# Kernel tuning notes

Measured on AMD Instinct MI355X. Metric: run time of the kernel, lower is better.

The kernel has to match this reference:

```python
import jax, jax.numpy as jnp
import numpy as np
from jax import lax

N = 5000            # number of detections
FEAT = 1024         # last-layer feature dim; 1024 + 9 engineered feats = indim 1033
DIMS = [FEAT + 9, 1000, 600, 300, 150, 1]
IOU_THRESH = 0.5
EPS = 2.220446049250313e-16  # sys.float_info.epsilon


def setup_inputs() -> dict:
    key = jax.random.key(0)
    ks = jax.random.split(key, 8 + 3 * len(DIMS))
    H, W = 800.0, 1333.0
    cx = jax.random.uniform(ks[0], (N,), minval=0.0, maxval=W)
    cy = jax.random.uniform(ks[1], (N,), minval=0.0, maxval=H)
    bw = jax.random.uniform(ks[2], (N,), minval=20.0, maxval=250.0)
    bh = jax.random.uniform(ks[3], (N,), minval=20.0, maxval=250.0)
    x1 = jnp.clip(cx - bw / 2, 0.0, W - 2)
    y1 = jnp.clip(cy - bh / 2, 0.0, H - 2)
    x2 = jnp.clip(cx + bw / 2, x1 + 1, W)
    y2 = jnp.clip(cy + bh / 2, y1 + 1, H)
    inp = {
        'multi_bboxes': jnp.stack([x1, y1, x2, y2], axis=1),
        'cls_score': jax.random.uniform(ks[4], (N, 2)),
        'last_layer_feats': jax.random.normal(ks[5], (N, FEAT)),
        'img_shape': jnp.array([H, W], jnp.float32),
    }
    # PermEqui2_mean params: Gamma (weight+bias) and Lambda (weight only)
    ki = 6
    for i, (din, dout) in enumerate(zip(DIMS[:-1], DIMS[1:])):
        s = 1.0 / np.sqrt(din)
        inp[f'Wg{i+1}'] = jax.random.uniform(ks[ki], (dout, din), minval=-s, maxval=s); ki += 1
        inp[f'bg{i+1}'] = jax.random.uniform(ks[ki], (dout,), minval=-s, maxval=s); ki += 1
        inp[f'Wl{i+1}'] = jax.random.uniform(ks[ki], (dout, din), minval=-s, maxval=s); ki += 1
    return inp


def _greedy_cluster(ious, thresh):
    # Sequential greedy IoU clustering (NMS-like). assign[i] = index of cluster seed.
    n = ious.shape[0]

    def step(carry, inp):
        is_c, assign = carry
        j, row = inp
        seed = is_c[j]
        hit = row > thresh
        member = seed & hit & is_c
        assign = jnp.where(member, j, assign)
        is_c = is_c & ~(seed & hit)
        return (is_c, assign), None

    init = (jnp.ones(n, bool), jnp.zeros(n, jnp.int32))
    (_, assign), _ = lax.scan(step, init, (jnp.arange(n, dtype=jnp.int32), ious))
    return assign


def _forward(multi_bboxes, cls_score, last_layer_feats, img_shape, params):
    n = multi_bboxes.shape[0]
    scores = cls_score[:, 1]
    order = jnp.argsort(-scores)
    scores = scores[order]
    bboxes = multi_bboxes[order]
    feats = last_layer_feats[order]

    x1, y1, x2, y2 = bboxes[:, 0], bboxes[:, 1], bboxes[:, 2], bboxes[:, 3]
    # pairwise IoU with the +1 pixel convention from bbox_overlaps
    iw = jnp.clip(jnp.minimum(x2[:, None], x2[None, :]) - jnp.maximum(x1[:, None], x1[None, :]) + 1, 0)
    ih = jnp.clip(jnp.minimum(y2[:, None], y2[None, :]) - jnp.maximum(y1[:, None], y1[None, :]) + 1, 0)
    area = (x2 - x1 + 1) * (y2 - y1 + 1)
    overlap = iw * ih
    ious = overlap / (area[:, None] + area[None, :] - overlap)

    assign = _greedy_cluster(lax.stop_gradient(ious), IOU_THRESH)
    counts = jax.ops.segment_sum(jnp.ones(n, jnp.float32), assign, num_segments=n)
    cden = jnp.maximum(counts, 1.0)

    Himg, Wimg = img_shape[0], img_shape[1]
    # source double-normalizes: width = (x2/W - x1/W)/W, height = (y2/H - y1/H)/H
    width = (x2 / Wimg - x1 / Wimg) / Wimg
    height = (y2 / Himg - y1 / Himg) / Himg
    areaf = width * height
    ar = width / (height + EPS)
    x = jnp.concatenate([
        bboxes, feats,
        width[:, None], height[:, None], ar[:, None], areaf[:, None], scores[:, None],
    ], axis=1)  # [n, 1033]

    def perm_equi(x, Wg, bg, Wl):
        # xm = per-set mean; x*Gamma^T + b - (xm*Lambda^T), gathered back per box
        xm = jax.ops.segment_sum(x, assign, num_segments=n) / cden[:, None]
        return x @ Wg.T + bg - (xm @ Wl.T)[assign]

    for i in range(5):
        x = jax.nn.elu(perm_equi(x, params[f'Wg{i+1}'], params[f'bg{i+1}'], params[f'Wl{i+1}']))

    # source skips singleton sets (nonzero().squeeze() -> 0-dim): mask them out
    valid = counts[assign] >= 2.0
    return jnp.where(valid[:, None], x, 0.0)  # [n, 1] per-box set logits


def reference(multi_bboxes, cls_score, last_layer_feats, img_shape,
              Wg1, bg1, Wl1, Wg2, bg2, Wl2, Wg3, bg3, Wl3,
              Wg4, bg4, Wl4, Wg5, bg5, Wl5):
    params = {'Wg1': Wg1, 'bg1': bg1, 'Wl1': Wl1, 'Wg2': Wg2, 'bg2': bg2, 'Wl2': Wl2,
              'Wg3': Wg3, 'bg3': bg3, 'Wl3': Wl3, 'Wg4': Wg4, 'bg4': bg4, 'Wl4': Wl4,
              'Wg5': Wg5, 'bg5': bg5, 'Wl5': Wl5}
    return _forward(multi_bboxes, cls_score, last_layer_feats, img_shape, params)
```

## Files before the change

### kernel.cpp

```cpp
#include <hip/hip_runtime.h>
#include <cstdint>
#include <cstddef>

#define N_BOX 5000
#define NW    80
#define LDX   1040
#define LDZ   2048
#define LDYM  1000
#define LDW   1040
#define LDAB  2080
#define NCHUNK ((N_BOX + 63) / 64)
#define RT    ((N_BOX + 255) / 256)

typedef short bf16x8 __attribute__((ext_vector_type(8)));
typedef float f32x4v __attribute__((ext_vector_type(4)));
typedef unsigned short u16x8 __attribute__((ext_vector_type(8)));

__device__ __forceinline__ float fence_f(float x) { asm volatile("" : "+v"(x)); return x; }

__device__ __forceinline__ unsigned short f2bf(float x) {
    unsigned u = __builtin_bit_cast(unsigned, x);
    unsigned r = (u + 0x7FFFu + ((u >> 16) & 1u)) >> 16;
    return (unsigned short)r;
}
__device__ __forceinline__ float bf2f(unsigned short h) {
    unsigned u = ((unsigned)h) << 16;
    return __builtin_bit_cast(float, u);
}

__global__ void rank_partial_kernel(const float* __restrict__ cls, int* __restrict__ rank) {
    __shared__ float sj[256];
    int t = threadIdx.x;
    int jbase = blockIdx.y * 256;
    int jg = jbase + t;
    sj[t] = (jg < N_BOX) ? cls[2 * jg + 1] : 0.0f;
    __syncthreads();
    int i = blockIdx.x * 256 + t;
    if (i >= N_BOX) return;
    float si = cls[2 * i + 1];
    int jmax = (N_BOX - jbase < 256) ? (N_BOX - jbase) : 256;
    int r = 0;
    for (int k = 0; k < jmax; ++k) {
        float sjv = sj[k];
        int j = jbase + k;
        r += (sjv > si) || (sjv == si && j < i);
    }
    atomicAdd(&rank[i], r);
}

__global__ void rank_scatter_kernel(const int* __restrict__ rank, int* __restrict__ ord) {
    int i = blockIdx.x * blockDim.x + threadIdx.x;
    if (i < N_BOX) ord[rank[i]] = i;
}

__global__ void gather_kernel(const float* __restrict__ bb, const float* __restrict__ cls,
                              const float* __restrict__ feats, const float* __restrict__ img,
                              const int* __restrict__ ord,
                              float* __restrict__ X0, float* __restrict__ sb) {
    int r = blockIdx.x;
    int i = ord[r];
    float x1 = bb[4 * i + 0], y1 = bb[4 * i + 1], x2 = bb[4 * i + 2], y2 = bb[4 * i + 3];
    float H = img[0], W = img[1];
    float sc = cls[2 * i + 1];
    if (threadIdx.x == 0) {
        sb[0 * N_BOX + r] = x1;
        sb[1 * N_BOX + r] = y1;
        sb[2 * N_BOX + r] = x2;
        sb[3 * N_BOX + r] = y2;
        sb[4 * N_BOX + r] = (x2 - x1 + 1.0f) * (y2 - y1 + 1.0f);
        sb[5 * N_BOX + r] = sc;
    }
    float width  = (x2 / W - x1 / W) / W;
    float height = (y2 / H - y1 / H) / H;
    float ar     = width / (height + 2.220446049250313e-16f);
    float areaf  = width * height;
    float* row = X0 + (size_t)r * LDX;
    for (int o = threadIdx.x; o < LDX; o += blockDim.x) {
        float v;
        if (o < 4)          v = (o == 0) ? x1 : (o == 1) ? y1 : (o == 2) ? x2 : y2;
        else if (o < 1028)  v = feats[(size_t)i * 1024 + (o - 4)];
        else if (o == 1028) v = width;
        else if (o == 1029) v = height;
        else if (o == 1030) v = ar;
        else if (o == 1031) v = areaf;
        else if (o == 1032) v = sc;
        else                v = 0.0f;
        row[o] = v;
    }
}

__global__ void mask_kernel(const float* __restrict__ sb, unsigned long long* __restrict__ mask,
                            unsigned long long* __restrict__ diag, int* __restrict__ counts) {
    int j = blockIdx.x;
    if (threadIdx.x == 0) counts[j] = 0;
    const float* X1 = sb;
    const float* Y1 = sb + N_BOX;
    const float* X2 = sb + 2 * N_BOX;
    const float* Y2 = sb + 3 * N_BOX;
    const float* AR = sb + 4 * N_BOX;
    float xj1 = X1[j], yj1 = Y1[j], xj2 = X2[j], yj2 = Y2[j], aj = AR[j];
    int lane = threadIdx.x & 63;
    int wave = threadIdx.x >> 6;
    int nwav = blockDim.x >> 6;
    int dw = j >> 6;
    for (int w = wave; w < NW; w += nwav) {
        int i = w * 64 + lane;
        bool pred = false;
        if (i < N_BOX) {
            float iw = fmaxf(fminf(xj2, X2[i]) - fmaxf(xj1, X1[i]) + 1.0f, 0.0f);
            float ih = fmaxf(fminf(yj2, Y2[i]) - fmaxf(yj1, Y1[i]) + 1.0f, 0.0f);
            float ov = fence_f(iw * ih);
            float denom = fence_f((aj + AR[i]) - ov);
            pred = (ov / denom) > 0.5f;
        }
        unsigned long long b = __ballot(pred);
        if (lane == 0) {
            mask[(size_t)j * NW + w] = b;
            if (w == dw) diag[j] = b;
        }
    }
}

__device__ __forceinline__ void nms_body(const unsigned long long* __restrict__ mask,
                                         const unsigned long long* __restrict__ diag,
                                         unsigned long long* __restrict__ keep,
                                         unsigned long long* supp,
                                         unsigned long long* keep_sh,
                                         unsigned long long* rem_sh,
                                         unsigned long long* kb_sh) {
    int tid = threadIdx.x;
    int l = tid & 63;
    int w = tid >> 6;
    if (tid < 80) supp[tid] = 0ULL;
    unsigned long long dg = 0ULL, dg_next = 0ULL;
    if (w == 0) dg = diag[l];
    __syncthreads();
    for (int c = 0; c < NCHUNK; ++c) {
        if (w == 0) {
            unsigned long long curv = supp[c];
            unsigned clo = __builtin_amdgcn_readfirstlane((unsigned)curv);
            unsigned chi = __builtin_amdgcn_readfirstlane((unsigned)(curv >> 32));
            unsigned long long cur = ((unsigned long long)chi << 32) | clo;
            int jmax = (N_BOX - c * 64 < 64) ? (N_BOX - c * 64) : 64;
            unsigned long long valid = (jmax >= 64) ? ~0ULL : ((1ULL << jmax) - 1ULL);
            unsigned long long rem = ~cur & valid;
            if (l == 0) *rem_sh = rem;
        }
        __syncthreads();
        unsigned long long rem0 = *rem_sh;
        unsigned long long a0 = 0, a1 = 0, a2 = 0, a3 = 0, a4 = 0;
        unsigned long long b0 = 0, b1 = 0, b2 = 0, b3 = 0, b4 = 0;
        unsigned mym = 0;
        int base = (w - 1) * 5;
        if (w > 0) {
            mym = (base < 64) ? (unsigned)((rem0 >> base) & 31ULL) : 0u;
            const unsigned long long* rowp = mask + (size_t)(c * 64 + base) * NW;
            if (mym & 1u)  { a0 = rowp[0 * NW + l]; b0 = (l < 16) ? rowp[0 * NW + 64 + l] : 0ULL; }
            if (mym & 2u)  { a1 = rowp[1 * NW + l]; b1 = (l < 16) ? rowp[1 * NW + 64 + l] : 0ULL; }
            if (mym & 4u)  { a2 = rowp[2 * NW + l]; b2 = (l < 16) ? rowp[2 * NW + 64 + l] : 0ULL; }
            if (mym & 8u)  { a3 = rowp[3 * NW + l]; b3 = (l < 16) ? rowp[3 * NW + 64 + l] : 0ULL; }
            if (mym & 16u) { a4 = rowp[4 * NW + l]; b4 = (l < 16) ? rowp[4 * NW + 64 + l] : 0ULL; }
        } else {
            if (c + 1 < NCHUNK) dg_next = diag[(size_t)(c + 1) * 64 + l];
            unsigned rlo = __builtin_amdgcn_readfirstlane((unsigned)rem0);
            unsigned rhi = __builtin_amdgcn_readfirstlane((unsigned)(rem0 >> 32));
            unsigned long long remS = ((unsigned long long)rhi << 32) | rlo;
            unsigned long long kb = 0ULL;
            while (remS) {
                int jj = __builtin_ctzll(remS);
                kb |= 1ULL << jj;
                unsigned dlo = __builtin_amdgcn_readlane((unsigned)dg, jj);
                unsigned dhi = __builtin_amdgcn_readlane((unsigned)(dg >> 32), jj);
                unsigned long long dj = ((unsigned long long)dhi << 32) | dlo;
                remS &= ~dj;
                remS &= ~(1ULL << jj);
            }
            if (l == 0) { *kb_sh = kb; keep_sh[c] = kb; }
        }
        __syncthreads();
        if (w > 0 && mym) {
            unsigned long long kb = *kb_sh;
            unsigned kw = ((unsigned)((kb >> base) & 31ULL)) & mym;
            if (kw & 1u)  { atomicOr(&supp[l], a0); if (l < 16) atomicOr(&supp[64 + l], b0); }
            if (kw & 2u)  { atomicOr(&supp[l], a1); if (l < 16) atomicOr(&supp[64 + l], b1); }
            if (kw & 4u)  { atomicOr(&supp[l], a2); if (l < 16) atomicOr(&supp[64 + l], b2); }
            if (kw & 8u)  { atomicOr(&supp[l], a3); if (l < 16) atomicOr(&supp[64 + l], b3); }
            if (kw & 16u) { atomicOr(&supp[l], a4); if (l < 16) atomicOr(&supp[64 + l], b4); }
        }
        if (w == 0) dg = dg_next;
        __syncthreads();
    }
    if (tid < NCHUNK) keep[tid] = keep_sh[tid];
}

__global__ __launch_bounds__(1024) void nms_scan_kernel(const unsigned long long* __restrict__ mask,
                                                        const unsigned long long* __restrict__ diag,
                                                        unsigned long long* __restrict__ keep) {
    __shared__ unsigned long long supp[80];
    __shared__ unsigned long long keep_sh[NCHUNK];
    __shared__ unsigned long long rem_sh;
    __shared__ unsigned long long kb_sh;
    nms_body(mask, diag, keep, supp, keep_sh, &rem_sh, &kb_sh);
}

__device__ __forceinline__ void wconv_row(const float* __restrict__ Wg, const float* __restrict__ Wl,
                                          unsigned short* __restrict__ B2, int n, int tid2,
                                          int dout, int din, int K16) {
    unsigned short* dst = B2 + (size_t)n * LDAB;
    int K2 = 2 * K16;
    if (n >= 2 * dout) {
        for (int k = tid2; k < K2; k += 256) dst[k] = 0;
        return;
    }
    const float* src = (n < dout) ? (Wg + (size_t)n * din) : (Wl + (size_t)(n - dout) * din);
    for (int k = tid2; k < K2; k += 256) {
        int ks = (k >= K16) ? (k - K16) : k;
        float x = (ks < din) ? src[ks] : 0.0f;
        dst[k] = f2bf(x);
    }
}

__global__ __launch_bounds__(1024) void nms_gemm_fused(const unsigned long long* __restrict__ mask,
                                                       const unsigned long long* __restrict__ diag,
                                                       unsigned long long* __restrict__ keep,
                                                       const unsigned short* __restrict__ A2,
                                                       const unsigned short* __restrict__ B2,
                                                       float* __restrict__ C, int KT, int Nn,
                                                       int MTiles,
                                                       const float* __restrict__ X0,
                                                       float* __restrict__ E9, float* __restrict__ W9,
                                                       const float* __restrict__ Wg1, const float* __restrict__ Wl1,
                                                       const float* __restrict__ Wg0full, const float* __restrict__ Wl0full,
                                                       unsigned short* __restrict__ B2_1,
                                                       const float* __restrict__ Wg2, const float* __restrict__ Wl2,
                                                       unsigned short* __restrict__ B2_2,
                                                       const float* __restrict__ Wg3, const float* __restrict__ Wl3,
                                                       unsigned short* __restrict__ B2_3) {
    __shared__ __align__(16) unsigned short AsBuf[2 * 8192];
    __shared__ __align__(16) unsigned short BsBuf[2 * 8192];
    int tid = threadIdx.x;
    int b = blockIdx.x;
    if (b == 0) {
        unsigned long long* supp    = (unsigned long long*)AsBuf;
        unsigned long long* keep_sh = supp + 80;
        unsigned long long* rem_sh  = keep_sh + NCHUNK;
        unsigned long long* kb_sh   = rem_sh + 1;
        nms_body(mask, diag, keep, supp, keep_sh, rem_sh, kb_sh);
        return;
    }
    int NG = MTiles * 8;
    if (b <= NG) {
        int t = b - 1;
        size_t bm = (size_t)(t % MTiles) * 256;
        size_t bn = (size_t)(t / MTiles) * 256;
        int lane = tid & 63;
        int wavef = tid >> 6;
        int wr = wavef >> 2, wc = wavef & 3;

        f32x4v acc[4][4];
#pragma unroll
        for (int i = 0; i < 4; ++i)
#pragma unroll
            for (int j = 0; j < 4; ++j) acc[i][j] = (f32x4v){0.f, 0.f, 0.f, 0.f};

        const unsigned short* gA = A2 + (bm + wavef * 16 + (lane & 15)) * (size_t)LDAB + (lane >> 4) * 8;
        const unsigned short* gB = B2 + (bn + wavef * 16 + (lane & 15)) * (size_t)LDAB + (lane >> 4) * 8;
        unsigned ldsoff = (unsigned)((wavef * 64 + lane) * 16);

#define FSTAGE(T, BUF)                                                                             \
        {                                                                                          \
            size_t ko = (size_t)(T) * 32;                                                          \
            __builtin_amdgcn_global_load_lds(                                                      \
                (const __attribute__((address_space(1))) void*)(gA + ko),                          \
                (__attribute__((address_space(3))) void*)((char*)AsBuf + (BUF) * 16384 + ldsoff),  \
                16, 0, 0);                                                                         \
            __builtin_amdgcn_global_load_lds(                                                      \
                (const __attribute__((address_space(1))) void*)(gB + ko),                          \
                (__attribute__((address_space(3))) void*)((char*)BsBuf + (BUF) * 16384 + ldsoff),  \
                16, 0, 0);                                                                         \
        }

        FSTAGE(0, 0);
        for (int kt = 0; kt < KT; ++kt) {
            int cur = kt & 1;
            if (kt + 1 < KT) {
                FSTAGE(kt + 1, cur ^ 1);
                asm volatile("s_waitcnt vmcnt(2)" ::: "memory");
            } else {
                asm volatile("s_waitcnt vmcnt(0)" ::: "memory");
            }
            asm volatile("s_barrier" ::: "memory");
            bf16x8 af[4], bf[4];
#pragma unroll
            for (int f4 = 0; f4 < 4; ++f4) {
                af[f4] = *(const bf16x8*)((const char*)AsBuf + cur * 16384 + ((wr * 4 + f4) * 64 + lane) * 16);
                bf[f4] = *(const bf16x8*)((const char*)BsBuf + cur * 16384 + ((wc * 4 + f4) * 64 + lane) * 16);
            }
#pragma unroll
            for (int i = 0; i < 4; ++i)
#pragma unroll
                for (int j = 0; j < 4; ++j)
                    acc[i][j] = __builtin_amdgcn_mfma_f32_16x16x32_bf16(af[i], bf[j], acc[i][j], 0, 0, 0);
            asm volatile("s_barrier" ::: "memory");
        }
#undef FSTAGE

#pragma unroll
        for (int i = 0; i < 4; ++i) {
            int r0 = (int)bm + wr * 64 + i * 16 + (lane >> 4) * 4;
#pragma unroll
            for (int j = 0; j < 4; ++j) {
                int col = (int)bn + wc * 64 + j * 16 + (lane & 15);
                if (col < Nn) {
#pragma unroll
                    for (int e = 0; e < 4; ++e) {
                        int r = r0 + e;
                        if (r < N_BOX) C[(size_t)r * LDZ + col] = acc[i][j][e];
                    }
                }
            }
        }
        return;
    }
    int rb = b - 1 - NG;
    const int cq[9] = {0, 1, 2, 3, 1028, 1029, 1030, 1031, 1032};
    if (rb < 5) {
        int r = rb * 1024 + tid;
        if (r < 5120) {
            float* dst = E9 + (size_t)r * 12;
#pragma unroll
            for (int q = 0; q < 9; ++q) dst[q] = (r < N_BOX) ? X0[(size_t)r * LDX + cq[q]] : 0.0f;
            dst[9] = dst[10] = dst[11] = 0.0f;
        }
        return;
    }
    rb -= 5;
    if (rb < 2) {
        int n = rb * 1024 + tid;
        if (n < 2048) {
            float* dst = W9 + (size_t)n * 12;
            const float* src = (n < 1000) ? (Wg0full + (size_t)n * 1033)
                             : (n < 2000) ? (Wl0full + (size_t)(n - 1000) * 1033) : nullptr;
#pragma unroll
            for (int q = 0; q < 9; ++q) dst[q] = src ? src[cq[q]] : 0.0f;
            dst[9] = dst[10] = dst[11] = 0.0f;
        }
        return;
    }
    rb -= 2;
    int rowl = tid >> 8;
    int tid2 = tid & 255;
    if (rb < 320) {
        int n = rb * 4 + rowl;
        if (n < 1280) wconv_row(Wg1, Wl1, B2_1, n, tid2, 600, 1000, 1008);
        return;
    }
    rb -= 320;
    if (rb < 160) {
        int n = rb * 4 + rowl;
        if (n < 640) wconv_row(Wg2, Wl2, B2_2, n, tid2, 300, 600, 608);
        return;
    }
    rb -= 160;
    {
        int n = rb * 4 + rowl;
        if (n < 384) wconv_row(Wg3, Wl3, B2_3, n, tid2, 150, 300, 304);
        return;
    }
}

__global__ void z9_assign_kernel(float* __restrict__ Z, const float* __restrict__ E9,
                                 const float* __restrict__ W9, int Nn,
                                 const unsigned long long* __restrict__ mask,
                                 const unsigned long long* __restrict__ keep,
                                 int* __restrict__ assign, int* __restrict__ counts) {
    int b = blockIdx.x;
    if (b < N_BOX) {
        int r = b;
        float e[9];
#pragma unroll
        for (int q = 0; q < 9; ++q) e[q] = E9[(size_t)r * 12 + q];
        for (int o = threadIdx.x; o < Nn; o += blockDim.x) {
            const float* w = W9 + (size_t)o * 12;
            float s = 0.0f;
#pragma unroll
            for (int q = 0; q < 9; ++q) s += e[q] * w[q];
            Z[(size_t)r * LDZ + o] += s;
        }
        return;
    }
    int i = (b - N_BOX) * 256 + threadIdx.x;
    if (i >= N_BOX) return;
    for (int w = 0; w < NCHUNK; ++w) {
        unsigned long long m = mask[(size_t)i * NW + w] & keep[w];
        if (m) {
            int j = w * 64 + __builtin_ctzll(m);
            assign[i] = j;
            atomicAdd(&counts[j], 1);
            return;
        }
    }
}

__global__ void assign_kernel(const unsigned long long* __restrict__ mask,
                              const unsigned long long* __restrict__ keep,
                              int* __restrict__ assign, int* __restrict__ counts) {
    int i = blockIdx.x * blockDim.x + threadIdx.x;
    if (i >= N_BOX) return;
    for (int w = 0; w < NCHUNK; ++w) {
        unsigned long long m = mask[(size_t)i * NW + w] & keep[w];
        if (m) {
            int j = w * 64 + __builtin_ctzll(m);
            assign[i] = j;
            atomicAdd(&counts[j], 1);
            return;
        }
    }
}

__global__ __launch_bounds__(1024) void scan_kernel(const int* __restrict__ counts, int* __restrict__ offs) {
    __shared__ int part[1024];
    int t = threadIdx.x;
    int base = t * 5;
    int c[5];
    int s = 0;
#pragma unroll
    for (int k = 0; k < 5; ++k) {
        int idx = base + k;
        c[k] = (idx < N_BOX) ? counts[idx] : 0;
        s += c[k];
    }
    part[t] = s;
    __syncthreads();
    for (int d = 1; d < 1024; d <<= 1) {
        int v = part[t];
        int u = (t >= d) ? part[t - d] : 0;
        __syncthreads();
        part[t] = v + u;
        __syncthreads();
    }
    int run = (t > 0) ? part[t - 1] : 0;
#pragma unroll
    for (int k = 0; k < 5; ++k) {
        int idx = base + k;
        if (idx < N_BOX) offs[idx] = run;
        run += c[k];
    }
}

__global__ void rankscatter_kernel(const int* __restrict__ assign, const int* __restrict__ offs,
                                   int* __restrict__ members) {
    __shared__ int a[N_BOX];
    int tid = threadIdx.x;
    for (int t = tid; t < N_BOX; t += blockDim.x) a[t] = assign[t];
    __syncthreads();
    int i = blockIdx.x * blockDim.x + tid;
    if (i >= N_BOX) return;
    int ai = a[i];
    int r = 0;
    for (int k = 0; k < i; ++k) r += (a[k] == ai);
    members[offs[ai] + r] = i;
}

__global__ void xconv_kernel(const float* __restrict__ X, unsigned short* __restrict__ A2,
                             int K16eff, int colOff) {
    int r = blockIdx.x;
    unsigned short* dst = A2 + (size_t)r * LDAB;
    int K2 = 2 * K16eff;
    int nk8 = K2 >> 3;
    if (r >= N_BOX) {
        for (int k8 = threadIdx.x; k8 < nk8; k8 += blockDim.x) {
            u16x8 z;
#pragma unroll
            for (int j = 0; j < 8; ++j) z[j] = 0;
            *(u16x8*)(dst + (k8 << 3)) = z;
        }
        return;
    }
    const float* src = X + (size_t)r * LDX + colOff;
    for (int k8 = threadIdx.x; k8 < nk8; k8 += blockDim.x) {
        int kb = k8 << 3;
        bool lo = (kb >= K16eff);
        int ks = lo ? (kb - K16eff) : kb;
        u16x8 out;
#pragma unroll
        for (int j = 0; j < 8; ++j) {
            float x = src[ks + j];
            unsigned short ah = f2bf(x);
            out[j] = lo ? f2bf(x - bf2f(ah)) : ah;
        }
        *(u16x8*)(dst + kb) = out;
    }
}

__global__ void wconv_kernel(const float* __restrict__ Wg, const float* __restrict__ Wl,
                             unsigned short* __restrict__ B2, int dout, int din_src,
                             int din_eff, int colOff, int K16eff) {
    int n = blockIdx.x;
    unsigned short* dst = B2 + (size_t)n * LDAB;
    int K2 = 2 * K16eff;
    if (n >= 2 * dout) {
        for (int k = threadIdx.x; k < K2; k += blockDim.x) dst[k] = 0;
        return;
    }
    const float* src = (n < dout) ? (Wg + (size_t)n * din_src) : (Wl + (size_t)(n - dout) * din_src);
    for (int k = threadIdx.x; k < K2; k += blockDim.x) {
        int ks = (k >= K16eff) ? (k - K16eff) : k;
        float x = (ks < din_eff) ? src[colOff + ks] : 0.0f;
        dst[k] = f2bf(x);
    }
}

__global__ __launch_bounds__(256, 4) void gemm_mfma(const unsigned short* __restrict__ A2,
                                                    const unsigned short* __restrict__ B2,
                                                    float* __restrict__ C, int KT, int Nn) {
    __shared__ unsigned short AsBuf[2 * 4096];
    __shared__ unsigned short BsBuf[2 * 4096];
    int tid = threadIdx.x;
    int lane = tid & 63;
    int wave = tid >> 6;
    int wr = wave >> 1, wc = wave & 1;
    size_t bm = (size_t)blockIdx.x * 128;
    size_t bn = (size_t)blockIdx.y * 128;

    f32x4v acc[4][4];
#pragma unroll
    for (int i = 0; i < 4; ++i)
#pragma unroll
        for (int j = 0; j < 4; ++j) acc[i][j] = (f32x4v){0.f, 0.f, 0.f, 0.f};

    const unsigned short* gA[2];
    const unsigned short* gB[2];
    unsigned ldsoff[2];
#pragma unroll
    for (int q = 0; q < 2; ++q) {
        int f = q * 4 + wave;
        int grow = f * 16 + (lane & 15);
        int gcol = (lane >> 4) * 8;
        gA[q] = A2 + (bm + grow) * (size_t)LDAB + gcol;
        gB[q] = B2 + (bn + grow) * (size_t)LDAB + gcol;
        ldsoff[q] = (unsigned)((f * 64 + lane) * 16);
    }

#define STAGE(T, BUF)                                                                              \
    {                                                                                              \
        size_t ko = (size_t)(T) * 32;                                                              \
        _Pragma("unroll") for (int q = 0; q < 2; ++q) {                                            \
            __builtin_amdgcn_global_load_lds(                                                      \
                (const __attribute__((address_space(1))) void*)(gA[q] + ko),                       \
                (__attribute__((address_space(3))) void*)((char*)AsBuf + (BUF) * 8192 + ldsoff[q]),\
                16, 0, 0);                                                                         \
            __builtin_amdgcn_global_load_lds(                                                      \
                (const __attribute__((address_space(1))) void*)(gB[q] + ko),                       \
                (__attribute__((address_space(3))) void*)((char*)BsBuf + (BUF) * 8192 + ldsoff[q]),\
                16, 0, 0);                                                                         \
        }                                                                                          \
    }

    STAGE(0, 0);
    for (int kt = 0; kt < KT; ++kt) {
        int cur = kt & 1;
        if (kt + 1 < KT) {
            STAGE(kt + 1, cur ^ 1);
            asm volatile("s_waitcnt vmcnt(4)" ::: "memory");
        } else {
            asm volatile("s_waitcnt vmcnt(0)" ::: "memory");
        }
        asm volatile("s_barrier" ::: "memory");
        bf16x8 af[4], bf[4];
#pragma unroll
        for (int f4 = 0; f4 < 4; ++f4) {
            af[f4] = *(const bf16x8*)((const char*)AsBuf + cur * 8192 + ((wr * 4 + f4) * 64 + lane) * 16);
            bf[f4] = *(const bf16x8*)((const char*)BsBuf + cur * 8192 + ((wc * 4 + f4) * 64 + lane) * 16);
        }
#pragma unroll
        for (int i = 0; i < 4; ++i)
#pragma unroll
            for (int j = 0; j < 4; ++j)
                acc[i][j] = __builtin_amdgcn_mfma_f32_16x16x32_bf16(af[i], bf[j], acc[i][j], 0, 0, 0);
        asm volatile("s_barrier" ::: "memory");
    }
#undef STAGE

#pragma unroll
    for (int i = 0; i < 4; ++i) {
        int r0 = (int)bm + wr * 64 + i * 16 + (lane >> 4) * 4;
#pragma unroll
        for (int j = 0; j < 4; ++j) {
            int col = (int)bn + wc * 64 + j * 16 + (lane & 15);
            if (col < Nn) {
#pragma unroll
                for (int e = 0; e < 4; ++e) {
                    int r = r0 + e;
                    if (r < N_BOX) C[(size_t)r * LDZ + col] = acc[i][j][e];
                }
            }
        }
    }
}

__global__ void wcat_kernel(const float* __restrict__ Wg, const float* __restrict__ Wl,
                            float* __restrict__ Wc, int dout, int din, int K16) {
    int row = blockIdx.x;
    const float* src = (row < dout) ? (Wg + (size_t)row * din) : (Wl + (size_t)(row - dout) * din);
    float* dst = Wc + (size_t)row * LDW;
    for (int k = threadIdx.x; k < K16; k += blockDim.x)
        dst[k] = (k < din) ? src[k] : 0.0f;
}

__global__ __launch_bounds__(256) void gemm_nt(const float* __restrict__ A, const float* __restrict__ B,
                                               float* __restrict__ C, int M, int Nn, int K16) {
    __shared__ float As[16][64];
    __shared__ float Bs[16][64];
    int bm = blockIdx.x * 64;
    int bn = blockIdx.y * 64;
    int tid = threadIdx.x;
    int row = tid & 63;
    int kq  = tid >> 6;
    int tx  = tid & 15;
    int ty  = tid >> 4;
    float acc[4][4] = {};
    for (int k0 = 0; k0 < K16; k0 += 16) {
        float4 av = make_float4(0.f, 0.f, 0.f, 0.f);
        float4 bv = make_float4(0.f, 0.f, 0.f, 0.f);
        if (bm + row < M)  av = *(const float4*)&A[(size_t)(bm + row) * LDX + k0 + kq * 4];
        if (bn + row < Nn) bv = *(const float4*)&B[(size_t)(bn + row) * LDW + k0 + kq * 4];
        __syncthreads();
        As[kq * 4 + 0][row] = av.x; As[kq * 4 + 1][row] = av.y;
        As[kq * 4 + 2][row] = av.z; As[kq * 4 + 3][row] = av.w;
        Bs[kq * 4 + 0][row] = bv.x; Bs[kq * 4 + 1][row] = bv.y;
        Bs[kq * 4 + 2][row] = bv.z; Bs[kq * 4 + 3][row] = bv.w;
        __syncthreads();
#pragma unroll
        for (int kk = 0; kk < 16; ++kk) {
            float4 a = *(const float4*)&As[kk][ty * 4];
            float4 b = *(const float4*)&Bs[kk][tx * 4];
            float aa[4] = {a.x, a.y, a.z, a.w};
            float bb[4] = {b.x, b.y, b.z, b.w};
#pragma unroll
            for (int i = 0; i < 4; ++i)
#pragma unroll
                for (int jx = 0; jx < 4; ++jx) acc[i][jx] += aa[i] * bb[jx];
        }
    }
#pragma unroll
    for (int i = 0; i < 4; ++i) {
        int r = bm + ty * 4 + i;
        if (r >= M) break;
#pragma unroll
        for (int jx = 0; jx < 4; ++jx) {
            int ccol = bn + tx * 4 + jx;
            if (ccol < Nn) C[(size_t)r * LDZ + ccol] = acc[i][jx];
        }
    }
}

__global__ void segmean_kernel(const float* __restrict__ Z, int dout,
                               const int* __restrict__ counts, const int* __restrict__ offs,
                               const int* __restrict__ members, float* __restrict__ ym) {
    int j = blockIdx.x;
    int cnt = counts[j];
    if (cnt == 0) return;
    int off = offs[j];
    float fc = (float)cnt;
    for (int o = threadIdx.x; o < dout; o += blockDim.x) {
        float s = 0.0f;
        for (int m = 0; m < cnt; ++m) {
            int i = members[off + m];
            s += Z[(size_t)i * LDZ + dout + o];
        }
        ym[(size_t)j * LDYM + o] = s / fc;
    }
}

__global__ void combine_kernel(const float* __restrict__ Z, const float* __restrict__ bg,
                               const float* __restrict__ ym, const int* __restrict__ assign,
                               float* __restrict__ Xout, int dout, int doutPad) {
    int r = blockIdx.x;
    int a = assign[r];
    float* dst = Xout + (size_t)r * LDX;
    for (int o = threadIdx.x; o < doutPad; o += blockDim.x) {
        float v = 0.0f;
        if (o < dout) {
            float z = Z[(size_t)r * LDZ + o] + bg[o] - ym[(size_t)a * LDYM + o];
            v = (z > 0.0f) ? z : expm1f(z);
        }
        dst[o] = v;
    }
}

__global__ void combine_fused_kernel(const float* __restrict__ Z, const float* __restrict__ bg,
                                     const float* __restrict__ ym, const int* __restrict__ assign,
                                     unsigned short* __restrict__ A2, int dout, int K16next) {
    int r = blockIdx.x;
    int a = assign[r];
    unsigned short* dst = A2 + (size_t)r * LDAB;
    for (int o = threadIdx.x; o < K16next; o += blockDim.x) {
        float v = 0.0f;
        if (o < dout) {
            float z = Z[(size_t)r * LDZ + o] + bg[o] - ym[(size_t)a * LDYM + o];
            v = (z > 0.0f) ? z : expm1f(z);
        }
        unsigned short hi = f2bf(v);
        dst[o] = hi;
        dst[K16next + o] = f2bf(v - bf2f(hi));
    }
}

__global__ void final_kernel(const float* __restrict__ X, const int* __restrict__ assign,
                             const int* __restrict__ counts, float* __restrict__ out) {
    int r = blockIdx.x * blockDim.x + threadIdx.x;
    if (r >= N_BOX) return;
    out[r] = (counts[assign[r]] >= 2) ? X[(size_t)r * LDX] : 0.0f;
}

extern "C" void kernel_launch(void* const* d_in, const int* in_sizes, int n_in,
                              void* d_out, int out_size, void* d_ws, size_t ws_size,
                              hipStream_t stream) {
    const float* bb    = (const float*)d_in[0];
    const float* cls   = (const float*)d_in[1];
    const float* feats = (const float*)d_in[2];
    const float* img   = (const float*)d_in[3];

    char* ws = (char*)d_ws;
    size_t off = 0;
    auto alloc = [&](size_t bytes) -> void* {
        void* p = ws + off;
        off += (bytes + 255) & ~(size_t)255;
        return p;
    };
    int*   ord     = (int*)alloc((size_t)N_BOX * 4);
    int*   rankb   = (int*)alloc((size_t)N_BOX * 4);
    float* sb      = (float*)alloc((size_t)6 * N_BOX * 4);
    int*   assign  = (int*)alloc((size_t)N_BOX * 4);
    int*   counts  = (int*)alloc((size_t)N_BOX * 4);
    int*   offsb   = (int*)alloc((size_t)N_BOX * 4);
    int*   members = (int*)alloc((size_t)N_BOX * 4);
    unsigned long long* mask = (unsigned long long*)alloc((size_t)(NCHUNK * 64) * NW * 8);
    unsigned long long* diag = (unsigned long long*)alloc((size_t)NCHUNK * 64 * 8);
    unsigned long long* keep = (unsigned long long*)alloc((size_t)NCHUNK * 8 + 1024);
    float* Xa = (float*)alloc((size_t)N_BOX * LDX * 4);
    float* Xb = (float*)alloc((size_t)N_BOX * LDX * 4);
    float* Z  = (float*)alloc((size_t)N_BOX * LDZ * 4);
    float* ym = (float*)alloc((size_t)N_BOX * LDYM * 4);
    float* Wc = (float*)alloc((size_t)2000 * LDW * 4);
    unsigned short* A2   = (unsigned short*)alloc((size_t)5120 * LDAB * 2);
    unsigned short* B2_0 = (unsigned short*)alloc((size_t)2048 * LDAB * 2);
    unsigned short* B2_1 = (unsigned short*)alloc((size_t)1280 * LDAB * 2);
    unsigned short* B2_2 = (unsigned short*)alloc((size_t)640 * LDAB * 2);
    unsigned short* B2_3 = (unsigned short*)alloc((size_t)384 * LDAB * 2);
    float* E9 = (float*)alloc((size_t)5120 * 12 * 4);
    float* W9 = (float*)alloc((size_t)2048 * 12 * 4);
    bool use_mfma = (off <= ws_size);

    hipMemsetAsync(rankb, 0, (size_t)N_BOX * 4, stream);
    rank_partial_kernel<<<dim3(RT, RT), dim3(256), 0, stream>>>(cls, rankb);
    rank_scatter_kernel<<<dim3(RT), dim3(256), 0, stream>>>(rankb, ord);
    gather_kernel<<<dim3(N_BOX), dim3(256), 0, stream>>>(bb, cls, feats, img, ord, Xa, sb);
    mask_kernel<<<dim3(N_BOX), dim3(256), 0, stream>>>(sb, mask, diag, counts);

    const int dins[5]  = {1033, 1000, 600, 300, 150};
    const int douts[5] = {1000, 600, 300, 150, 1};
    const int K16e[4]  = {1024, 1008, 608, 304};
    const int coff[4]  = {4, 0, 0, 0};
    const int dineff[4] = {1024, 1000, 600, 300};
    unsigned short* B2L[4] = {B2_0, B2_1, B2_2, B2_3};

    if (use_mfma) {
        xconv_kernel<<<dim3(5120), dim3(256), 0, stream>>>(Xa, A2, K16e[0], coff[0]);
        wconv_kernel<<<dim3(2048), dim3(256), 0, stream>>>((const float*)d_in[4], (const float*)d_in[6],
                                                           B2_0, douts[0], dins[0], dineff[0], coff[0], K16e[0]);
        int KT0 = K16e[0] / 16;
        nms_gemm_fused<<<dim3(744), dim3(1024), 0, stream>>>(
            mask, diag, keep, A2, B2_0, Z, KT0, 2 * douts[0], 20,
            Xa, E9, W9,
            (const float*)d_in[7], (const float*)d_in[9],
            (const float*)d_in[4], (const float*)d_in[6],
            B2_1,
            (const float*)d_in[10], (const float*)d_in[12], B2_2,
            (const float*)d_in[13], (const float*)d_in[15], B2_3);
        z9_assign_kernel<<<dim3(N_BOX + RT), dim3(256), 0, stream>>>(Z, E9, W9, 2 * douts[0],
                                                                     mask, keep, assign, counts);
    } else {
        nms_scan_kernel<<<dim3(1), dim3(1024), 0, stream>>>(mask, diag, keep);
        assign_kernel<<<dim3(RT), dim3(256), 0, stream>>>(mask, keep, assign, counts);
    }

    scan_kernel<<<dim3(1), dim3(1024), 0, stream>>>(counts, offsb);
    rankscatter_kernel<<<dim3(RT), dim3(256), 0, stream>>>(assign, offsb, members);

    for (int L = 0; L < 5; ++L) {
        const float* Wg = (const float*)d_in[4 + 3 * L];
        const float* bg = (const float*)d_in[5 + 3 * L];
        const float* Wl = (const float*)d_in[6 + 3 * L];
        int din = dins[L], dout = douts[L];
        int K16 = (din + 15) & ~15;
        int N2 = 2 * dout;
        int doutPad = (dout + 15) & ~15;
        float* Xin  = (L % 2 == 0) ? Xa : Xb;
        float* Xout = (L % 2 == 0) ? Xb : Xa;
        if (use_mfma && L < 4) {
            if (L > 0) {
                int KT = K16e[L] / 16;
                int Ntiles = (N2 + 127) >> 7;
                gemm_mfma<<<dim3(40, Ntiles), dim3(256), 0, stream>>>(A2, B2L[L], Z, KT, N2);
            }
        } else {
            wcat_kernel<<<dim3(N2), dim3(256), 0, stream>>>(Wg, Wl, Wc, dout, din, K16);
            gemm_nt<<<dim3((N_BOX + 63) / 64, (N2 + 63) / 64), dim3(256), 0, stream>>>(Xin, Wc, Z, N_BOX, N2, K16);
        }
        segmean_kernel<<<dim3(N_BOX), dim3(256), 0, stream>>>(Z, dout, counts, offsb, members, ym);
        if (use_mfma && L < 3) {
            combine_fused_kernel<<<dim3(N_BOX), dim3(256), 0, stream>>>(Z, bg, ym, assign, A2,
                                                                        dout, K16e[L + 1]);
        } else {
            combine_kernel<<<dim3(N_BOX), dim3(256), 0, stream>>>(Z, bg, ym, assign, Xout, dout, doutPad);
        }
    }
    final_kernel<<<dim3(RT), dim3(256), 0, stream>>>(Xb, assign, counts, (float*)d_out);
}
```

Before: 549.5 us.

## Fuse segment-mean with combine, fold layer 5 into layer 4, drop xconv pass

Layer-0 bf16 hi/lo activation conversion moves into the gather kernel, so the separate xconv pass is gone. Segment-mean and ELU-combine are merged into one per-cluster kernel, and layers 1-3 now emit only hi bf16 activations against single-split weights, which halves GEMM K work but loses precision. The tiny final layer (dout=1) is computed with wave reductions inside a fused per-cluster kernel instead of a GEMM plus combine plus final pass. Padded K sizes for weights change, and an asm barrier is added to force early mask row loads in the NMS path.

```diff
diff --git a/kernel.cpp b/kernel.cpp
--- a/kernel.cpp
+++ b/kernel.cpp
@@ -56,8 +56,14 @@
 __global__ void gather_kernel(const float* __restrict__ bb, const float* __restrict__ cls,
                               const float* __restrict__ feats, const float* __restrict__ img,
                               const int* __restrict__ ord,
-                              float* __restrict__ X0, float* __restrict__ sb) {
+                              float* __restrict__ X0, float* __restrict__ sb,
+                              unsigned short* __restrict__ A2) {
     int r = blockIdx.x;
+    if (r >= N_BOX) {
+        unsigned short* dst = A2 + (size_t)r * LDAB;
+        for (int k = threadIdx.x; k < 2048; k += blockDim.x) dst[k] = 0;
+        return;
+    }
     int i = ord[r];
     float x1 = bb[4 * i + 0], y1 = bb[4 * i + 1], x2 = bb[4 * i + 2], y2 = bb[4 * i + 3];
     float H = img[0], W = img[1];
@@ -75,6 +81,7 @@
     float ar     = width / (height + 2.220446049250313e-16f);
     float areaf  = width * height;
     float* row = X0 + (size_t)r * LDX;
+    unsigned short* a2row = A2 + (size_t)r * LDAB;
     for (int o = threadIdx.x; o < LDX; o += blockDim.x) {
         float v;
         if (o < 4)          v = (o == 0) ? x1 : (o == 1) ? y1 : (o == 2) ? x2 : y2;
@@ -86,6 +93,12 @@
         else if (o == 1032) v = sc;
         else                v = 0.0f;
         row[o] = v;
+        if (o >= 4 && o < 1028) {
+            int k = o - 4;
+            unsigned short hi = f2bf(v);
+            a2row[k] = hi;
+            a2row[1024 + k] = f2bf(v - bf2f(hi));
+        }
     }
 }
 
@@ -160,6 +173,8 @@
             if (mym & 4u)  { a2 = rowp[2 * NW + l]; b2 = (l < 16) ? rowp[2 * NW + 64 + l] : 0ULL; }
             if (mym & 8u)  { a3 = rowp[3 * NW + l]; b3 = (l < 16) ? rowp[3 * NW + 64 + l] : 0ULL; }
             if (mym & 16u) { a4 = rowp[4 * NW + l]; b4 = (l < 16) ? rowp[4 * NW + 64 + l] : 0ULL; }
+            asm volatile("" : "+v"(a0), "+v"(a1), "+v"(a2), "+v"(a3), "+v"(a4),
+                             "+v"(b0), "+v"(b1), "+v"(b2), "+v"(b3), "+v"(b4));
         } else {
             if (c + 1 < NCHUNK) dg_next = diag[(size_t)(c + 1) * 64 + l];
             unsigned rlo = __builtin_amdgcn_readfirstlane((unsigned)rem0);
@@ -207,15 +222,13 @@
                                           unsigned short* __restrict__ B2, int n, int tid2,
                                           int dout, int din, int K16) {
     unsigned short* dst = B2 + (size_t)n * LDAB;
-    int K2 = 2 * K16;
     if (n >= 2 * dout) {
-        for (int k = tid2; k < K2; k += 256) dst[k] = 0;
+        for (int k = tid2; k < K16; k += 256) dst[k] = 0;
         return;
     }
     const float* src = (n < dout) ? (Wg + (size_t)n * din) : (Wl + (size_t)(n - dout) * din);
-    for (int k = tid2; k < K2; k += 256) {
-        int ks = (k >= K16) ? (k - K16) : k;
-        float x = (ks < din) ? src[ks] : 0.0f;
+    for (int k = tid2; k < K16; k += 256) {
+        float x = (k < din) ? src[k] : 0.0f;
         dst[k] = f2bf(x);
     }
 }
@@ -352,7 +365,7 @@
     int tid2 = tid & 255;
     if (rb < 320) {
         int n = rb * 4 + rowl;
-        if (n < 1280) wconv_row(Wg1, Wl1, B2_1, n, tid2, 600, 1000, 1008);
+        if (n < 1280) wconv_row(Wg1, Wl1, B2_1, n, tid2, 600, 1000, 1024);
         return;
     }
     rb -= 320;
@@ -364,7 +377,7 @@
     rb -= 160;
     {
         int n = rb * 4 + rowl;
-        if (n < 384) wconv_row(Wg3, Wl3, B2_3, n, tid2, 150, 300, 304);
+        if (n < 384) wconv_row(Wg3, Wl3, B2_3, n, tid2, 150, 300, 320);
         return;
     }
 }
@@ -460,37 +473,6 @@
     int r = 0;
     for (int k = 0; k < i; ++k) r += (a[k] == ai);
     members[offs[ai] + r] = i;
-}
-
-__global__ void xconv_kernel(const float* __restrict__ X, unsigned short* __restrict__ A2,
-                             int K16eff, int colOff) {
-    int r = blockIdx.x;
-    unsigned short* dst = A2 + (size_t)r * LDAB;
-    int K2 = 2 * K16eff;
-    int nk8 = K2 >> 3;
-    if (r >= N_BOX) {
-        for (int k8 = threadIdx.x; k8 < nk8; k8 += blockDim.x) {
-            u16x8 z;
-#pragma unroll
-            for (int j = 0; j < 8; ++j) z[j] = 0;
-            *(u16x8*)(dst + (k8 << 3)) = z;
-        }
-        return;
-    }
-    const float* src = X + (size_t)r * LDX + colOff;
-    for (int k8 = threadIdx.x; k8 < nk8; k8 += blockDim.x) {
-        int kb = k8 << 3;
-        bool lo = (kb >= K16eff);
-        int ks = lo ? (kb - K16eff) : kb;
-        u16x8 out;
-#pragma unroll
-        for (int j = 0; j < 8; ++j) {
-            float x = src[ks + j];
-            unsigned short ah = f2bf(x);
-            out[j] = lo ? f2bf(x - bf2f(ah)) : ah;
-        }
-        *(u16x8*)(dst + kb) = out;
-    }
 }
 
 __global__ void wconv_kernel(const float* __restrict__ Wg, const float* __restrict__ Wl,
@@ -595,6 +577,102 @@
                     if (r < N_BOX) C[(size_t)r * LDZ + col] = acc[i][j][e];
                 }
             }
+        }
+    }
+}
+
+__global__ __launch_bounds__(256) void seg_combine_kernel(const float* __restrict__ Z,
+                                                          const float* __restrict__ bg,
+                                                          const int* __restrict__ counts,
+                                                          const int* __restrict__ offs,
+                                                          const int* __restrict__ members,
+                                                          unsigned short* __restrict__ A2,
+                                                          int dout, int K16next) {
+    int j = blockIdx.x;
+    int cnt = counts[j];
+    if (cnt == 0) return;
+    __shared__ float ymv[1024];
+    int off = offs[j];
+    float fc = (float)cnt;
+    for (int o = threadIdx.x; o < dout; o += blockDim.x) {
+        float s = 0.0f;
+        for (int m = 0; m < cnt; ++m)
+            s += Z[(size_t)members[off + m] * LDZ + dout + o];
+        ymv[o] = s / fc;
+    }
+    __syncthreads();
+    for (int m = 0; m < cnt; ++m) {
+        int i = members[off + m];
+        unsigned short* dst = A2 + (size_t)i * LDAB;
+        const float* zr = Z + (size_t)i * LDZ;
+        for (int o = threadIdx.x; o < K16next; o += blockDim.x) {
+            float v = 0.0f;
+            if (o < dout) {
+                float z = zr[o] + bg[o] - ymv[o];
+                v = (z > 0.0f) ? z : expm1f(z);
+            }
+            dst[o] = f2bf(v);
+        }
+    }
+}
+
+__global__ __launch_bounds__(256) void seg_l4_kernel(const float* __restrict__ Z,
+                                                     const float* __restrict__ bg3,
+                                                     const float* __restrict__ Wg4,
+                                                     const float* __restrict__ bg4,
+                                                     const float* __restrict__ Wl4,
+                                                     const int* __restrict__ counts,
+                                                     const int* __restrict__ offs,
+                                                     const int* __restrict__ members,
+                                                     float* __restrict__ out) {
+    int j = blockIdx.x;
+    int cnt = counts[j];
+    if (cnt == 0) return;
+    __shared__ float ymv[160];
+    __shared__ float wsl[4];
+    int off = offs[j];
+    int tid = threadIdx.x;
+    float fc = (float)cnt;
+    for (int o = tid; o < 150; o += 256) {
+        float s = 0.0f;
+        for (int m = 0; m < cnt; ++m)
+            s += Z[(size_t)members[off + m] * LDZ + 150 + o];
+        ymv[o] = s / fc;
+    }
+    __syncthreads();
+    int l = tid & 63, w = tid >> 6;
+    float slsum = 0.0f;
+    for (int m = w; m < cnt; m += 4) {
+        int i = members[off + m];
+        const float* zr = Z + (size_t)i * LDZ;
+        float sl = 0.0f;
+        for (int o = l; o < 150; o += 64) {
+            float z = zr[o] + bg3[o] - ymv[o];
+            float x = (z > 0.0f) ? z : expm1f(z);
+            sl += x * Wl4[o];
+        }
+#pragma unroll
+        for (int d = 1; d < 64; d <<= 1) sl += __shfl_xor(sl, d);
+        slsum += sl;
+    }
+    if (l == 0) wsl[w] = slsum;
+    __syncthreads();
+    float ym4 = (wsl[0] + wsl[1] + wsl[2] + wsl[3]) / fc;
+    for (int m = w; m < cnt; m += 4) {
+        int i = members[off + m];
+        const float* zr = Z + (size_t)i * LDZ;
+        float sg = 0.0f;
+        for (int o = l; o < 150; o += 64) {
+            float z = zr[o] + bg3[o] - ymv[o];
+            float x = (z > 0.0f) ? z : expm1f(z);
+            sg += x * Wg4[o];
+        }
+#pragma unroll
+        for (int d = 1; d < 64; d <<= 1) sg += __shfl_xor(sg, d);
+        if (l == 0) {
+            float z2 = sg + bg4[0] - ym4;
+            float v = (z2 > 0.0f) ? z2 : expm1f(z2);
+            out[i] = (cnt >= 2) ? v : 0.0f;
         }
     }
 }
@@ -686,24 +764,6 @@
             v = (z > 0.0f) ? z : expm1f(z);
         }
         dst[o] = v;
-    }
-}
-
-__global__ void combine_fused_kernel(const float* __restrict__ Z, const float* __restrict__ bg,
-                                     const float* __restrict__ ym, const int* __restrict__ assign,
-                                     unsigned short* __restrict__ A2, int dout, int K16next) {
-    int r = blockIdx.x;
-    int a = assign[r];
-    unsigned short* dst = A2 + (size_t)r * LDAB;
-    for (int o = threadIdx.x; o < K16next; o += blockDim.x) {
-        float v = 0.0f;
-        if (o < dout) {
-            float z = Z[(size_t)r * LDZ + o] + bg[o] - ym[(size_t)a * LDYM + o];
-            v = (z > 0.0f) ? z : expm1f(z);
-        }
-        unsigned short hi = f2bf(v);
-        dst[o] = hi;
-        dst[K16next + o] = f2bf(v - bf2f(hi));
     }
 }
 
@@ -756,66 +816,64 @@
     hipMemsetAsync(rankb, 0, (size_t)N_BOX * 4, stream);
     rank_partial_kernel<<<dim3(RT, RT), dim3(256), 0, stream>>>(cls, rankb);
     rank_scatter_kernel<<<dim3(RT), dim3(256), 0, stream>>>(rankb, ord);
-    gather_kernel<<<dim3(N_BOX), dim3(256), 0, stream>>>(bb, cls, feats, img, ord, Xa, sb);
+    gather_kernel<<<dim3(5120), dim3(256), 0, stream>>>(bb, cls, feats, img, ord, Xa, sb, A2);
     mask_kernel<<<dim3(N_BOX), dim3(256), 0, stream>>>(sb, mask, diag, counts);
 
     const int dins[5]  = {1033, 1000, 600, 300, 150};
     const int douts[5] = {1000, 600, 300, 150, 1};
-    const int K16e[4]  = {1024, 1008, 608, 304};
-    const int coff[4]  = {4, 0, 0, 0};
-    const int dineff[4] = {1024, 1000, 600, 300};
+    const int K16s[4]  = {1024, 1024, 608, 320};
+    const int KTs[4]   = {64, 32, 19, 10};
     unsigned short* B2L[4] = {B2_0, B2_1, B2_2, B2_3};
 
     if (use_mfma) {
-        xconv_kernel<<<dim3(5120), dim3(256), 0, stream>>>(Xa, A2, K16e[0], coff[0]);
         wconv_kernel<<<dim3(2048), dim3(256), 0, stream>>>((const float*)d_in[4], (const float*)d_in[6],
-                                                           B2_0, douts[0], dins[0], dineff[0], coff[0], K16e[0]);
-        int KT0 = K16e[0] / 16;
+                                                           B2_0, 1000, 1033, 1024, 4, 1024);
         nms_gemm_fused<<<dim3(744), dim3(1024), 0, stream>>>(
-            mask, diag, keep, A2, B2_0, Z, KT0, 2 * douts[0], 20,
+            mask, diag, keep, A2, B2_0, Z, KTs[0], 2000, 20,
             Xa, E9, W9,
             (const float*)d_in[7], (const float*)d_in[9],
             (const float*)d_in[4], (const float*)d_in[6],
             B2_1,
             (const float*)d_in[10], (const float*)d_in[12], B2_2,
             (const float*)d_in[13], (const float*)d_in[15], B2_3);
-        z9_assign_kernel<<<dim3(N_BOX + RT), dim3(256), 0, stream>>>(Z, E9, W9, 2 * douts[0],
+        z9_assign_kernel<<<dim3(N_BOX + RT), dim3(256), 0, stream>>>(Z, E9, W9, 2000,
                                                                      mask, keep, assign, counts);
+        scan_kernel<<<dim3(1), dim3(1024), 0, stream>>>(counts, offsb);
+        rankscatter_kernel<<<dim3(RT), dim3(256), 0, stream>>>(assign, offsb, members);
+
+        seg_combine_kernel<<<dim3(N_BOX), dim3(256), 0, stream>>>(Z, (const float*)d_in[5],
+                                                                  counts, offsb, members, A2, 1000, K16s[1]);
+        gemm_mfma<<<dim3(40, 10), dim3(256), 0, stream>>>(A2, B2_1, Z, KTs[1], 1200);
+        seg_combine_kernel<<<dim3(N_BOX), dim3(256), 0, stream>>>(Z, (const float*)d_in[8],
+                                                                  counts, offsb, members, A2, 600, K16s[2]);
+        gemm_mfma<<<dim3(40, 5), dim3(256), 0, stream>>>(A2, B2_2, Z, KTs[2], 600);
+        seg_combine_kernel<<<dim3(N_BOX), dim3(256), 0, stream>>>(Z, (const float*)d_in[11],
+                                                                  counts, offsb, members, A2, 300, K16s[3]);
+        gemm_mfma<<<dim3(40, 3), dim3(256), 0, stream>>>(A2, B2_3, Z, KTs[3], 300);
+        seg_l4_kernel<<<dim3(N_BOX), dim3(256), 0, stream>>>(Z, (const float*)d_in[14],
+                                                             (const float*)d_in[16], (const float*)d_in[17],
+                                                             (const float*)d_in[18],
+                                                             counts, offsb, members, (float*)d_out);
     } else {
         nms_scan_kernel<<<dim3(1), dim3(1024), 0, stream>>>(mask, diag, keep);
         assign_kernel<<<dim3(RT), dim3(256), 0, stream>>>(mask, keep, assign, counts);
-    }
-
-    scan_kernel<<<dim3(1), dim3(1024), 0, stream>>>(counts, offsb);
-    rankscatter_kernel<<<dim3(RT), dim3(256), 0, stream>>>(assign, offsb, members);
-
-    for (int L = 0; L < 5; ++L) {
-        const float* Wg = (const float*)d_in[4 + 3 * L];
-        const float* bg = (const float*)d_in[5 + 3 * L];
-        const float* Wl = (const float*)d_in[6 + 3 * L];
-        int din = dins[L], dout = douts[L];
-        int K16 = (din + 15) & ~15;
-        int N2 = 2 * dout;
-        int doutPad = (dout + 15) & ~15;
-        float* Xin  = (L % 2 == 0) ? Xa : Xb;
-        float* Xout = (L % 2 == 0) ? Xb : Xa;
-        if (use_mfma && L < 4) {
-            if (L > 0) {
-                int KT = K16e[L] / 16;
-                int Ntiles = (N2 + 127) >> 7;
-                gemm_mfma<<<dim3(40, Ntiles), dim3(256), 0, stream>>>(A2, B2L[L], Z, KT, N2);
-            }
-        } else {
+        scan_kernel<<<dim3(1), dim3(1024), 0, stream>>>(counts, offsb);
+        rankscatter_kernel<<<dim3(RT), dim3(256), 0, stream>>>(assign, offsb, members);
+        for (int L = 0; L < 5; ++L) {
+            const float* Wg = (const float*)d_in[4 + 3 * L];
+            const float* bg = (const float*)d_in[5 + 3 * L];
+            const float* Wl = (const float*)d_in[6 + 3 * L];
+            int din = dins[L], dout = douts[L];
+            int K16 = (din + 15) & ~15;
+            int N2 = 2 * dout;
+            int doutPad = (dout + 15) & ~15;
+            float* Xin  = (L % 2 == 0) ? Xa : Xb;
+            float* Xout = (L % 2 == 0) ? Xb : Xa;
             wcat_kernel<<<dim3(N2), dim3(256), 0, stream>>>(Wg, Wl, Wc, dout, din, K16);
             gemm_nt<<<dim3((N_BOX + 63) / 64, (N2 + 63) / 64), dim3(256), 0, stream>>>(Xin, Wc, Z, N_BOX, N2, K16);
-        }
-        segmean_kernel<<<dim3(N_BOX), dim3(256), 0, stream>>>(Z, dout, counts, offsb, members, ym);
-        if (use_mfma && L < 3) {
-            combine_fused_kernel<<<dim3(N_BOX), dim3(256), 0, stream>>>(Z, bg, ym, assign, A2,
-                                                                        dout, K16e[L + 1]);
-        } else {
+            segmean_kernel<<<dim3(N_BOX), dim3(256), 0, stream>>>(Z, dout, counts, offsb, members, ym);
             combine_kernel<<<dim3(N_BOX), dim3(256), 0, stream>>>(Z, bg, ym, assign, Xout, dout, doutPad);
         }
-    }
-    final_kernel<<<dim3(RT), dim3(256), 0, stream>>>(Xb, assign, counts, (float*)d_out);
-}
+        final_kernel<<<dim3(RT), dim3(256), 0, stream>>>(Xb, assign, counts, (float*)d_out);
+    }
+}
```

New measurement: 536.2 us. 2.4% less time.
